# Kernel optimization log

Hardware: AMD Instinct MI355X
Metric: run time of the kernel (lower is better)

Reference implementation:

```python
import jax, jax.numpy as jnp
import numpy as np

THRESH = 0.7
MIN_KEPT = 100000
IGNORE_INDEX = -100


def setup_inputs() -> dict:
    key = jax.random.key(0)
    k1, k2 = jax.random.split(key)
    B, C, H, W = 8, 19, 512, 512
    logits = jax.random.normal(k1, (B, C, H, W), dtype=jnp.float32)
    targets = jax.random.randint(k2, (B, H, W), 0, C, dtype=jnp.int64)
    return {"logits": logits, "targets": targets}


def reference(logits, targets):
    B, C, H, W = logits.shape
    # softmax over class dim, then log(p + eps) as in the original
    probs = jax.nn.softmax(logits, axis=1)
    log_probs = jnp.log(probs + 1e-7)
    mask = (targets != IGNORE_INDEX)
    # per-pixel NLL: gather log-prob of the target class
    gathered = jnp.take_along_axis(log_probs, targets[:, None, :, :], axis=1)[:, 0]  # [B,H,W]
    losses = -gathered * mask.astype(logits.dtype)                                   # [B,H,W]
    losses_flat = losses.reshape(B, -1)                                              # [B,HW]
    n_pix = losses_flat.shape[1]
    # threshold index is static (Python ints), matching torch code exactly
    thresh_idx = max(MIN_KEPT, int(n_pix * THRESH))
    thresh_idx = min(thresh_idx, n_pix - 1)
    sorted_losses = jnp.sort(losses_flat, axis=1)
    thresh = sorted_losses[:, thresh_idx]                                            # [B]
    selected = losses_flat > thresh[:, None]                                         # [B,HW] bool
    # Faithful to the original (buggy-looking) loop:
    #   selected_mask[i, targets[i].flatten()] = 1
    # i.e. target *values* are used as indices into the flattened HW axis.
    tgt_flat = targets.reshape(B, -1)  # values in [0, C)
    selected = jax.vmap(lambda s, t: s.at[t].set(True))(selected, tgt_flat)
    return selected.reshape(B, H, W).astype(jnp.float32)
```

## Files before the change

kernel.cpp:

```cpp
#include <hip/hip_runtime.h>

#define NB 8
#define NC 19
#define HW (512*512)
#define NPIX (NB*HW)
#define HHW (HW/2)
#define RANK 183500u
#define NBIN 4096
#define CAP  4096
#define OFFB 69696

__device__ __forceinline__ unsigned fkey(float f) {
    unsigned b = __float_as_uint(f);
    return (b & 0x80000000u) ? ~b : (b | 0x80000000u);
}
__device__ __forceinline__ float finv(unsigned u) {
    unsigned b = (u & 0x80000000u) ? (u & 0x7fffffffu) : ~u;
    return __uint_as_float(b);
}
__device__ __forceinline__ int bin_of(float l) {
    int b = (int)((l + 1.0f) * 224.0f);
    return b < 0 ? 0 : (b > NBIN - 1 ? NBIN - 1 : b);
}
__device__ __forceinline__ unsigned umn(unsigned a, unsigned b) { return a < b ? a : b; }
__device__ __forceinline__ unsigned umx(unsigned a, unsigned b) { return a > b ? a : b; }

__global__ __launch_bounds__(256) void losses_kernel(
    const float* __restrict__ logits, const int* __restrict__ targets,
    float* __restrict__ losses, unsigned* __restrict__ wszero)
{
    const int blk = blockIdx.x, tid = threadIdx.x;
    if (blk < 33) {
        int j = blk * 1024 + tid * 4;
        if (j < 32784) *reinterpret_cast<uint4*>(wszero + j) = make_uint4(0u,0u,0u,0u);
    }
    const int b  = blk >> 9;
    const int r  = ((blk & 511) << 8) + tid;
    const int rB = (r + OFFB) & (HHW - 1);
    const int pA = (b << 18) + r;
    const int pB = (b << 18) + HHW + rB;
    const float* cb = logits + (size_t)b * NC * HW;
    const int*   tb = targets + (size_t)b * HW;
    const unsigned vA = (unsigned)(r * 4);
    const unsigned vB = (unsigned)((HHW + rB) * 4);

    int tA, tB;
    float xA[NC], xB[NC];
    asm volatile("global_load_dword %0, %1, %2" : "=v"(tA) : "v"(vA), "s"(tb));
    asm volatile("global_load_dword %0, %1, %2" : "=v"(tB) : "v"(vB), "s"(tb));
    #pragma unroll
    for (int c = 0; c < NC; ++c)
        asm volatile("global_load_dword %0, %1, %2"
                     : "=v"(xA[c]) : "v"(vA), "s"(cb + (size_t)c * HW));
    #pragma unroll
    for (int c = 0; c < NC; ++c)
        asm volatile("global_load_dword %0, %1, %2"
                     : "=v"(xB[c]) : "v"(vB), "s"(cb + (size_t)c * HW));

    asm volatile("s_waitcnt vmcnt(19)" ::: "memory");
    __builtin_amdgcn_sched_barrier(0);

    {
        float m = xA[0];
        #pragma unroll
        for (int c = 1; c < NC; ++c) m = fmaxf(m, xA[c]);
        float s = 0.f, et = 0.f;
        #pragma unroll
        for (int c = 0; c < NC; ++c) {
            float e = expf(xA[c] - m);
            s += e;
            if (c == tA) et = e;
        }
        losses[pA] = (tA >= 0 && tA < NC) ? -logf(et / s + 1e-7f) : 0.f;
    }

    __builtin_amdgcn_sched_barrier(0);
    asm volatile("s_waitcnt vmcnt(1)" ::: "memory");
    __builtin_amdgcn_sched_barrier(0);

    {
        float m = xB[0];
        #pragma unroll
        for (int c = 1; c < NC; ++c) m = fmaxf(m, xB[c]);
        float s = 0.f, et = 0.f;
        #pragma unroll
        for (int c = 0; c < NC; ++c) {
            float e = expf(xB[c] - m);
            s += e;
            if (c == tB) et = e;
        }
        losses[pB] = (tB >= 0 && tB < NC) ? -logf(et / s + 1e-7f) : 0.f;
    }
}

__global__ __launch_bounds__(256) void hist_kernel(
    const float* __restrict__ losses, const int* __restrict__ targets,
    unsigned* __restrict__ ghist, unsigned* __restrict__ present)
{
    __shared__ unsigned lh[NBIN];
    __shared__ unsigned pres;
    const int b = blockIdx.y;
    for (int j = threadIdx.x; j < NBIN; j += 256) lh[j] = 0;
    if (threadIdx.x == 0) pres = 0u;
    __syncthreads();
    const float4* L = reinterpret_cast<const float4*>(losses + (size_t)b * HW)
                      + (size_t)blockIdx.x * 1024;
    const int4* T = reinterpret_cast<const int4*>(targets + (size_t)b * HW)
                    + (size_t)blockIdx.x * 1024;
    unsigned bits = 0u;
    for (int j = threadIdx.x; j < 1024; j += 256) {
        float4 v = L[j];
        atomicAdd(&lh[bin_of(v.x)], 1u);
        atomicAdd(&lh[bin_of(v.y)], 1u);
        atomicAdd(&lh[bin_of(v.z)], 1u);
        atomicAdd(&lh[bin_of(v.w)], 1u);
        int4 tv = T[j];
        if (tv.x >= 0 && tv.x < NC) bits |= 1u << tv.x;
        if (tv.y >= 0 && tv.y < NC) bits |= 1u << tv.y;
        if (tv.z >= 0 && tv.z < NC) bits |= 1u << tv.z;
        if (tv.w >= 0 && tv.w < NC) bits |= 1u << tv.w;
    }
    #pragma unroll
    for (int o = 1; o < 64; o <<= 1) bits |= __shfl_xor(bits, o);
    if ((threadIdx.x & 63) == 0 && bits) atomicOr(&pres, bits);
    __syncthreads();
    unsigned* gh = ghist + b * NBIN;
    for (int j = threadIdx.x; j < NBIN; j += 256) {
        unsigned v = lh[j];
        if (v) atomicAdd(&gh[j], v);
    }
    if (threadIdx.x == 0 && pres) atomicOr(&present[b], pres);
}

__global__ __launch_bounds__(256) void compact_kernel(
    const float* __restrict__ losses, const unsigned* __restrict__ ghist,
    unsigned* __restrict__ count, float* __restrict__ cand,
    unsigned* __restrict__ info)
{
    __shared__ unsigned wsum[4], woff[4];
    __shared__ unsigned sh_T, sh_r;
    const int b = blockIdx.y;
    const int tid = threadIdx.x;
    const int lane = tid & 63, wid = tid >> 6;
    const unsigned* gh = ghist + b * NBIN;

    unsigned s = 0;
    #pragma unroll
    for (int j = 0; j < 16; ++j) s += gh[tid * 16 + j];
    unsigned incl = s;
    #pragma unroll
    for (int o = 1; o < 64; o <<= 1) {
        unsigned v = (unsigned)__shfl_up((int)incl, o);
        if (lane >= o) incl += v;
    }
    if (lane == 63) wsum[wid] = incl;
    __syncthreads();
    if (tid == 0) { unsigned c = 0; for (int w = 0; w < 4; ++w) { woff[w] = c; c += wsum[w]; } }
    __syncthreads();
    unsigned excl = woff[wid] + incl - s;
    if (RANK >= excl && RANK < excl + s) {
        unsigned rr = RANK - excl, cum = 0;
        for (int j = 0; j < 16; ++j) {
            unsigned c = gh[tid * 16 + j];
            if (cum + c > rr) {
                sh_T = (unsigned)(tid * 16 + j); sh_r = rr - cum;
                if (blockIdx.x == 0) { info[b * 2] = sh_T; info[b * 2 + 1] = sh_r; }
                break;
            }
            cum += c;
        }
    }
    __syncthreads();
    const int T = (int)sh_T;

    const float4* L = reinterpret_cast<const float4*>(losses + (size_t)b * HW)
                      + (size_t)blockIdx.x * 1024;
    for (int j = tid; j < 1024; j += 256) {
        float4 v = L[j];
        float vals[4] = {v.x, v.y, v.z, v.w};
        #pragma unroll
        for (int q = 0; q < 4; ++q) {
            float val = vals[q];
            bool sel = (bin_of(val) == T);
            unsigned long long msk = __ballot(sel);
            if (msk) {
                int leader = __ffsll(msk) - 1;
                int pre = __popcll(msk & ((1ull << lane) - 1ull));
                unsigned base = 0;
                if (lane == leader) base = atomicAdd(&count[b], (unsigned)__popcll(msk));
                base = (unsigned)__shfl((int)base, leader);
                if (sel) {
                    unsigned idx = base + (unsigned)pre;
                    if (idx < CAP) cand[b * CAP + idx] = val;
                }
            }
        }
    }
}

__global__ __launch_bounds__(256) void final_kernel(
    const float* __restrict__ cand, const unsigned* __restrict__ count,
    const unsigned* __restrict__ info, float* __restrict__ thresh)
{
    __shared__ unsigned kf[CAP];
    __shared__ unsigned h[512];
    __shared__ unsigned sub[2048];
    __shared__ unsigned red[8];
    __shared__ unsigned kmin_sh, shift_sh, sb_sh, r2_sh, cnt_sh;
    const int tid = threadIdx.x, b = blockIdx.x;
    unsigned k = count[b]; if (k > CAP) k = CAP;
    const unsigned r = info[b * 2 + 1];

    for (unsigned j = tid; j < k; j += 256) kf[j] = fkey(cand[b * CAP + j]);
    for (int j = tid; j < 512; j += 256) h[j] = 0;
    __syncthreads();

    unsigned lmin = 0xFFFFFFFFu, lmax = 0u;
    for (unsigned j = tid; j < k; j += 256) { unsigned v = kf[j]; lmin = umn(lmin, v); lmax = umx(lmax, v); }
    #pragma unroll
    for (int o = 1; o < 64; o <<= 1) {
        lmin = umn(lmin, (unsigned)__shfl_xor((int)lmin, o));
        lmax = umx(lmax, (unsigned)__shfl_xor((int)lmax, o));
    }
    if ((tid & 63) == 0) { red[tid >> 6] = lmin; red[4 + (tid >> 6)] = lmax; }
    __syncthreads();
    if (tid == 0) {
        unsigned mn = red[0], mx = red[4];
        for (int w = 1; w < 4; ++w) { mn = umn(mn, red[w]); mx = umx(mx, red[4 + w]); }
        unsigned spread = mx - mn;
        int bits = 32 - __clz((int)(spread | 1u));
        shift_sh = (unsigned)(bits > 9 ? bits - 9 : 0);
        kmin_sh = mn;
        cnt_sh = 0;
    }
    __syncthreads();
    const unsigned kmin = kmin_sh, shift = shift_sh;
    for (unsigned j = tid; j < k; j += 256) atomicAdd(&h[(kf[j] - kmin) >> shift], 1u);
    __syncthreads();
    if (tid == 0) {
        unsigned cum = 0; int sb = 0;
        while (sb < 511 && cum + h[sb] <= r) { cum += h[sb]; ++sb; }
        sb_sh = (unsigned)sb; r2_sh = r - cum;
    }
    __syncthreads();
    const unsigned sb = sb_sh;
    for (unsigned j = tid; j < k; j += 256) {
        if (((kf[j] - kmin) >> shift) == sb) {
            unsigned idx = atomicAdd(&cnt_sh, 1u);
            if (idx < 2048) sub[idx] = kf[j];
        }
    }
    __syncthreads();
    const unsigned k2 = umn(cnt_sh, 2048u), r2 = r2_sh;
    for (unsigned e = tid; e < k2; e += 256) {
        unsigned v = sub[e], less = 0, eq = 0;
        for (unsigned j = 0; j < k2; ++j) { unsigned u = sub[j]; less += (u < v); eq += (u == v); }
        if (less <= r2 && r2 < less + eq) thresh[b] = finv(v);
    }
}

__global__ __launch_bounds__(256) void emit_kernel(
    float* __restrict__ out, const float* __restrict__ thresh,
    const unsigned* __restrict__ present)
{
    int i4 = blockIdx.x * 256 + threadIdx.x;
    int i = i4 * 4;
    int b = i >> 18;
    int p = i & (HW - 1);
    float th = thresh[b];
    unsigned pm = present[b];
    float4 v = reinterpret_cast<float4*>(out)[i4];
    float4 o;
    o.x = ((v.x > th) || ((p + 0) < NC && ((pm >> (p + 0)) & 1u))) ? 1.f : 0.f;
    o.y = ((v.y > th) || ((p + 1) < NC && ((pm >> (p + 1)) & 1u))) ? 1.f : 0.f;
    o.z = ((v.z > th) || ((p + 2) < NC && ((pm >> (p + 2)) & 1u))) ? 1.f : 0.f;
    o.w = ((v.w > th) || ((p + 3) < NC && ((pm >> (p + 3)) & 1u))) ? 1.f : 0.f;
    reinterpret_cast<float4*>(out)[i4] = o;
}

extern "C" void kernel_launch(void* const* d_in, const int* in_sizes, int n_in,
                              void* d_out, int out_size, void* d_ws, size_t ws_size,
                              hipStream_t stream)
{
    const float* logits  = (const float*)d_in[0];
    const int*   targets = (const int*)d_in[1];
    float* out = (float*)d_out;

    char* ws = (char*)d_ws;
    unsigned* ghist   = (unsigned*)(ws);
    unsigned* count   = (unsigned*)(ws + 131072);
    unsigned* present = (unsigned*)(ws + 131104);
    unsigned* info    = (unsigned*)(ws + 131136);
    float*    thresh  = (float*)   (ws + 131200);
    float*    cand    = (float*)   (ws + 131232);


    losses_kernel<<<NPIX / 512, 256, 0, stream>>>(logits, targets, out, ghist);
    hist_kernel<<<dim3(64, NB), 256, 0, stream>>>(out, targets, ghist, present);
    compact_kernel<<<dim3(64, NB), 256, 0, stream>>>(out, ghist, count, cand, info);
    final_kernel<<<NB, 256, 0, stream>>>(cand, count, info, thresh);
    emit_kernel<<<NPIX / 4 / 256, 256, 0, stream>>>(out, thresh, present);
}
```

Baseline: 106.1 us.

## Fuse histogram, compaction, selection and emit into one cooperative kernel

Replaces the four tail kernels with a single cooperative kernel that uses grid-wide syncs between phases. Each block loads its loss tile into registers once and reuses it for histogramming, candidate compaction and final mask emission, so the separate global re-reads of losses disappear. It also cuts three kernel launches and their gaps. The cost is three grid-wide barriers, a serial final phase running on only 8 blocks while the others wait, and the requirement that all 512 blocks stay co-resident.

```diff
diff --git a/kernel.cpp b/kernel.cpp
--- a/kernel.cpp
+++ b/kernel.cpp
@@ -1,4 +1,6 @@
 #include <hip/hip_runtime.h>
+#include <hip/hip_cooperative_groups.h>
+namespace cg = cooperative_groups;
 
 #define NB 8
 #define NC 19
@@ -93,28 +95,43 @@
     }
 }
 
-__global__ __launch_bounds__(256) void hist_kernel(
+__global__ __launch_bounds__(256, 3) void tail_kernel(
     const float* __restrict__ losses, const int* __restrict__ targets,
-    unsigned* __restrict__ ghist, unsigned* __restrict__ present)
+    float* __restrict__ out,
+    unsigned* __restrict__ ghist, unsigned* __restrict__ count,
+    unsigned* __restrict__ present, unsigned* __restrict__ info,
+    float* __restrict__ thresh, float* __restrict__ cand)
 {
     __shared__ unsigned lh[NBIN];
-    __shared__ unsigned pres;
-    const int b = blockIdx.y;
-    for (int j = threadIdx.x; j < NBIN; j += 256) lh[j] = 0;
-    if (threadIdx.x == 0) pres = 0u;
+    __shared__ unsigned h2[512];
+    __shared__ unsigned sub[2048];
+    __shared__ unsigned red[8];
+    __shared__ unsigned wsum[4], woff[4];
+    __shared__ unsigned sh_T, sh_kmin, sh_shift, sh_sb, sh_r2, sh_cnt, pres;
+
+    const int blk = blockIdx.x, tid = threadIdx.x;
+    cg::grid_group grid = cg::this_grid();
+    const int b    = blk >> 6;
+    const int cblk = blk & 63;
+    const int lane = tid & 63, wid = tid >> 6;
+
+    for (int j = tid; j < NBIN; j += 256) lh[j] = 0;
+    if (tid == 0) pres = 0u;
     __syncthreads();
-    const float4* L = reinterpret_cast<const float4*>(losses + (size_t)b * HW)
-                      + (size_t)blockIdx.x * 1024;
-    const int4* T = reinterpret_cast<const int4*>(targets + (size_t)b * HW)
-                    + (size_t)blockIdx.x * 1024;
+    const float4* Lp = reinterpret_cast<const float4*>(losses + (size_t)b * HW)
+                       + (size_t)cblk * 1024;
+    const int4*   Tp = reinterpret_cast<const int4*>(targets + (size_t)b * HW)
+                       + (size_t)cblk * 1024;
+    float4 L[4];
     unsigned bits = 0u;
-    for (int j = threadIdx.x; j < 1024; j += 256) {
-        float4 v = L[j];
-        atomicAdd(&lh[bin_of(v.x)], 1u);
-        atomicAdd(&lh[bin_of(v.y)], 1u);
-        atomicAdd(&lh[bin_of(v.z)], 1u);
-        atomicAdd(&lh[bin_of(v.w)], 1u);
-        int4 tv = T[j];
+    #pragma unroll
+    for (int it = 0; it < 4; ++it) {
+        L[it] = Lp[it * 256 + tid];
+        int4 tv = Tp[it * 256 + tid];
+        atomicAdd(&lh[bin_of(L[it].x)], 1u);
+        atomicAdd(&lh[bin_of(L[it].y)], 1u);
+        atomicAdd(&lh[bin_of(L[it].z)], 1u);
+        atomicAdd(&lh[bin_of(L[it].w)], 1u);
         if (tv.x >= 0 && tv.x < NC) bits |= 1u << tv.x;
         if (tv.y >= 0 && tv.y < NC) bits |= 1u << tv.y;
         if (tv.z >= 0 && tv.z < NC) bits |= 1u << tv.z;
@@ -122,160 +139,140 @@
     }
     #pragma unroll
     for (int o = 1; o < 64; o <<= 1) bits |= __shfl_xor(bits, o);
-    if ((threadIdx.x & 63) == 0 && bits) atomicOr(&pres, bits);
+    if ((tid & 63) == 0 && bits) atomicOr(&pres, bits);
     __syncthreads();
-    unsigned* gh = ghist + b * NBIN;
-    for (int j = threadIdx.x; j < NBIN; j += 256) {
-        unsigned v = lh[j];
-        if (v) atomicAdd(&gh[j], v);
-    }
-    if (threadIdx.x == 0 && pres) atomicOr(&present[b], pres);
-}
-
-__global__ __launch_bounds__(256) void compact_kernel(
-    const float* __restrict__ losses, const unsigned* __restrict__ ghist,
-    unsigned* __restrict__ count, float* __restrict__ cand,
-    unsigned* __restrict__ info)
-{
-    __shared__ unsigned wsum[4], woff[4];
-    __shared__ unsigned sh_T, sh_r;
-    const int b = blockIdx.y;
-    const int tid = threadIdx.x;
-    const int lane = tid & 63, wid = tid >> 6;
-    const unsigned* gh = ghist + b * NBIN;
-
-    unsigned s = 0;
-    #pragma unroll
-    for (int j = 0; j < 16; ++j) s += gh[tid * 16 + j];
-    unsigned incl = s;
-    #pragma unroll
-    for (int o = 1; o < 64; o <<= 1) {
-        unsigned v = (unsigned)__shfl_up((int)incl, o);
-        if (lane >= o) incl += v;
-    }
-    if (lane == 63) wsum[wid] = incl;
-    __syncthreads();
-    if (tid == 0) { unsigned c = 0; for (int w = 0; w < 4; ++w) { woff[w] = c; c += wsum[w]; } }
-    __syncthreads();
-    unsigned excl = woff[wid] + incl - s;
-    if (RANK >= excl && RANK < excl + s) {
-        unsigned rr = RANK - excl, cum = 0;
-        for (int j = 0; j < 16; ++j) {
-            unsigned c = gh[tid * 16 + j];
-            if (cum + c > rr) {
-                sh_T = (unsigned)(tid * 16 + j); sh_r = rr - cum;
-                if (blockIdx.x == 0) { info[b * 2] = sh_T; info[b * 2 + 1] = sh_r; }
-                break;
+    {
+        unsigned* gh = ghist + b * NBIN;
+        for (int j = tid; j < NBIN; j += 256) {
+            unsigned v = lh[j];
+            if (v) atomicAdd(&gh[j], v);
+        }
+        if (tid == 0 && pres) atomicOr(&present[b], pres);
+    }
+    grid.sync();
+
+    {
+        const unsigned* gh = ghist + b * NBIN;
+        unsigned s = 0;
+        #pragma unroll
+        for (int j = 0; j < 16; ++j) s += gh[tid * 16 + j];
+        unsigned incl = s;
+        #pragma unroll
+        for (int o = 1; o < 64; o <<= 1) {
+            unsigned v = (unsigned)__shfl_up((int)incl, o);
+            if (lane >= o) incl += v;
+        }
+        if (lane == 63) wsum[wid] = incl;
+        __syncthreads();
+        if (tid == 0) { unsigned c = 0; for (int w = 0; w < 4; ++w) { woff[w] = c; c += wsum[w]; } }
+        __syncthreads();
+        unsigned excl = woff[wid] + incl - s;
+        if (RANK >= excl && RANK < excl + s) {
+            unsigned rr = RANK - excl, cum = 0;
+            for (int j = 0; j < 16; ++j) {
+                unsigned c = gh[tid * 16 + j];
+                if (cum + c > rr) {
+                    sh_T = (unsigned)(tid * 16 + j);
+                    if (cblk == 0) { info[b * 2] = sh_T; info[b * 2 + 1] = rr - cum; }
+                    break;
+                }
+                cum += c;
             }
-            cum += c;
-        }
-    }
-    __syncthreads();
-    const int T = (int)sh_T;
-
-    const float4* L = reinterpret_cast<const float4*>(losses + (size_t)b * HW)
-                      + (size_t)blockIdx.x * 1024;
-    for (int j = tid; j < 1024; j += 256) {
-        float4 v = L[j];
-        float vals[4] = {v.x, v.y, v.z, v.w};
-        #pragma unroll
-        for (int q = 0; q < 4; ++q) {
-            float val = vals[q];
-            bool sel = (bin_of(val) == T);
-            unsigned long long msk = __ballot(sel);
-            if (msk) {
-                int leader = __ffsll(msk) - 1;
-                int pre = __popcll(msk & ((1ull << lane) - 1ull));
-                unsigned base = 0;
-                if (lane == leader) base = atomicAdd(&count[b], (unsigned)__popcll(msk));
-                base = (unsigned)__shfl((int)base, leader);
-                if (sel) {
-                    unsigned idx = base + (unsigned)pre;
-                    if (idx < CAP) cand[b * CAP + idx] = val;
+        }
+        __syncthreads();
+        const int T = (int)sh_T;
+        #pragma unroll
+        for (int it = 0; it < 4; ++it) {
+            float vals[4] = {L[it].x, L[it].y, L[it].z, L[it].w};
+            #pragma unroll
+            for (int q = 0; q < 4; ++q) {
+                float val = vals[q];
+                bool sel = (bin_of(val) == T);
+                unsigned long long msk = __ballot(sel);
+                if (msk) {
+                    int leader = __ffsll(msk) - 1;
+                    int pre = __popcll(msk & ((1ull << lane) - 1ull));
+                    unsigned base = 0;
+                    if (lane == leader) base = atomicAdd(&count[b], (unsigned)__popcll(msk));
+                    base = (unsigned)__shfl((int)base, leader);
+                    if (sel) {
+                        unsigned idx = base + (unsigned)pre;
+                        if (idx < CAP) cand[b * CAP + idx] = val;
+                    }
                 }
             }
         }
     }
-}
-
-__global__ __launch_bounds__(256) void final_kernel(
-    const float* __restrict__ cand, const unsigned* __restrict__ count,
-    const unsigned* __restrict__ info, float* __restrict__ thresh)
-{
-    __shared__ unsigned kf[CAP];
-    __shared__ unsigned h[512];
-    __shared__ unsigned sub[2048];
-    __shared__ unsigned red[8];
-    __shared__ unsigned kmin_sh, shift_sh, sb_sh, r2_sh, cnt_sh;
-    const int tid = threadIdx.x, b = blockIdx.x;
-    unsigned k = count[b]; if (k > CAP) k = CAP;
-    const unsigned r = info[b * 2 + 1];
-
-    for (unsigned j = tid; j < k; j += 256) kf[j] = fkey(cand[b * CAP + j]);
-    for (int j = tid; j < 512; j += 256) h[j] = 0;
-    __syncthreads();
-
-    unsigned lmin = 0xFFFFFFFFu, lmax = 0u;
-    for (unsigned j = tid; j < k; j += 256) { unsigned v = kf[j]; lmin = umn(lmin, v); lmax = umx(lmax, v); }
-    #pragma unroll
-    for (int o = 1; o < 64; o <<= 1) {
-        lmin = umn(lmin, (unsigned)__shfl_xor((int)lmin, o));
-        lmax = umx(lmax, (unsigned)__shfl_xor((int)lmax, o));
-    }
-    if ((tid & 63) == 0) { red[tid >> 6] = lmin; red[4 + (tid >> 6)] = lmax; }
-    __syncthreads();
-    if (tid == 0) {
-        unsigned mn = red[0], mx = red[4];
-        for (int w = 1; w < 4; ++w) { mn = umn(mn, red[w]); mx = umx(mx, red[4 + w]); }
-        unsigned spread = mx - mn;
-        int bits = 32 - __clz((int)(spread | 1u));
-        shift_sh = (unsigned)(bits > 9 ? bits - 9 : 0);
-        kmin_sh = mn;
-        cnt_sh = 0;
-    }
-    __syncthreads();
-    const unsigned kmin = kmin_sh, shift = shift_sh;
-    for (unsigned j = tid; j < k; j += 256) atomicAdd(&h[(kf[j] - kmin) >> shift], 1u);
-    __syncthreads();
-    if (tid == 0) {
-        unsigned cum = 0; int sb = 0;
-        while (sb < 511 && cum + h[sb] <= r) { cum += h[sb]; ++sb; }
-        sb_sh = (unsigned)sb; r2_sh = r - cum;
-    }
-    __syncthreads();
-    const unsigned sb = sb_sh;
-    for (unsigned j = tid; j < k; j += 256) {
-        if (((kf[j] - kmin) >> shift) == sb) {
-            unsigned idx = atomicAdd(&cnt_sh, 1u);
-            if (idx < 2048) sub[idx] = kf[j];
-        }
-    }
-    __syncthreads();
-    const unsigned k2 = umn(cnt_sh, 2048u), r2 = r2_sh;
-    for (unsigned e = tid; e < k2; e += 256) {
-        unsigned v = sub[e], less = 0, eq = 0;
-        for (unsigned j = 0; j < k2; ++j) { unsigned u = sub[j]; less += (u < v); eq += (u == v); }
-        if (less <= r2 && r2 < less + eq) thresh[b] = finv(v);
-    }
-}
-
-__global__ __launch_bounds__(256) void emit_kernel(
-    float* __restrict__ out, const float* __restrict__ thresh,
-    const unsigned* __restrict__ present)
-{
-    int i4 = blockIdx.x * 256 + threadIdx.x;
-    int i = i4 * 4;
-    int b = i >> 18;
-    int p = i & (HW - 1);
-    float th = thresh[b];
-    unsigned pm = present[b];
-    float4 v = reinterpret_cast<float4*>(out)[i4];
-    float4 o;
-    o.x = ((v.x > th) || ((p + 0) < NC && ((pm >> (p + 0)) & 1u))) ? 1.f : 0.f;
-    o.y = ((v.y > th) || ((p + 1) < NC && ((pm >> (p + 1)) & 1u))) ? 1.f : 0.f;
-    o.z = ((v.z > th) || ((p + 2) < NC && ((pm >> (p + 2)) & 1u))) ? 1.f : 0.f;
-    o.w = ((v.w > th) || ((p + 3) < NC && ((pm >> (p + 3)) & 1u))) ? 1.f : 0.f;
-    reinterpret_cast<float4*>(out)[i4] = o;
+    grid.sync();
+
+    if (blk < 8) {
+        const int fb = blk;
+        unsigned k = count[fb]; if (k > CAP) k = CAP;
+        const unsigned r = info[fb * 2 + 1];
+        for (unsigned j = tid; j < k; j += 256) lh[j] = fkey(cand[fb * CAP + j]);
+        for (int j = tid; j < 512; j += 256) h2[j] = 0;
+        __syncthreads();
+        unsigned lmin = 0xFFFFFFFFu, lmax = 0u;
+        for (unsigned j = tid; j < k; j += 256) { unsigned v = lh[j]; lmin = umn(lmin, v); lmax = umx(lmax, v); }
+        #pragma unroll
+        for (int o = 1; o < 64; o <<= 1) {
+            lmin = umn(lmin, (unsigned)__shfl_xor((int)lmin, o));
+            lmax = umx(lmax, (unsigned)__shfl_xor((int)lmax, o));
+        }
+        if ((tid & 63) == 0) { red[tid >> 6] = lmin; red[4 + (tid >> 6)] = lmax; }
+        __syncthreads();
+        if (tid == 0) {
+            unsigned mn = red[0], mx = red[4];
+            for (int w = 1; w < 4; ++w) { mn = umn(mn, red[w]); mx = umx(mx, red[4 + w]); }
+            unsigned spread = mx - mn;
+            int bits2 = 32 - __clz((int)(spread | 1u));
+            sh_shift = (unsigned)(bits2 > 9 ? bits2 - 9 : 0);
+            sh_kmin = mn;
+            sh_cnt = 0;
+        }
+        __syncthreads();
+        const unsigned kmin = sh_kmin, shift = sh_shift;
+        for (unsigned j = tid; j < k; j += 256) atomicAdd(&h2[(lh[j] - kmin) >> shift], 1u);
+        __syncthreads();
+        if (tid == 0) {
+            unsigned cum = 0; int sb = 0;
+            while (sb < 511 && cum + h2[sb] <= r) { cum += h2[sb]; ++sb; }
+            sh_sb = (unsigned)sb; sh_r2 = r - cum;
+        }
+        __syncthreads();
+        const unsigned sb = sh_sb;
+        for (unsigned j = tid; j < k; j += 256) {
+            if (((lh[j] - kmin) >> shift) == sb) {
+                unsigned idx = atomicAdd(&sh_cnt, 1u);
+                if (idx < 2048) sub[idx] = lh[j];
+            }
+        }
+        __syncthreads();
+        const unsigned k2 = umn(sh_cnt, 2048u), r2 = sh_r2;
+        for (unsigned e = tid; e < k2; e += 256) {
+            unsigned v = sub[e], less = 0, eq = 0;
+            for (unsigned j = 0; j < k2; ++j) { unsigned u = sub[j]; less += (u < v); eq += (u == v); }
+            if (less <= r2 && r2 < less + eq) thresh[fb] = finv(v);
+        }
+    }
+    grid.sync();
+
+    {
+        const float th = thresh[b];
+        const unsigned pm = present[b];
+        float4* Op = reinterpret_cast<float4*>(out + (size_t)b * HW)
+                     + (size_t)cblk * 1024;
+        #pragma unroll
+        for (int it = 0; it < 4; ++it) {
+            const int p0 = (cblk * 1024 + it * 256 + tid) * 4;
+            float4 o;
+            o.x = ((L[it].x > th) || ((p0 + 0) < NC && ((pm >> (p0 + 0)) & 1u))) ? 1.f : 0.f;
+            o.y = ((L[it].y > th) || ((p0 + 1) < NC && ((pm >> (p0 + 1)) & 1u))) ? 1.f : 0.f;
+            o.z = ((L[it].z > th) || ((p0 + 2) < NC && ((pm >> (p0 + 2)) & 1u))) ? 1.f : 0.f;
+            o.w = ((L[it].w > th) || ((p0 + 3) < NC && ((pm >> (p0 + 3)) & 1u))) ? 1.f : 0.f;
+            Op[it * 256 + tid] = o;
+        }
+    }
 }
 
 extern "C" void kernel_launch(void* const* d_in, const int* in_sizes, int n_in,
@@ -296,8 +293,11 @@
 
 
     losses_kernel<<<NPIX / 512, 256, 0, stream>>>(logits, targets, out, ghist);
-    hist_kernel<<<dim3(64, NB), 256, 0, stream>>>(out, targets, ghist, present);
-    compact_kernel<<<dim3(64, NB), 256, 0, stream>>>(out, ghist, count, cand, info);
-    final_kernel<<<NB, 256, 0, stream>>>(cand, count, info, thresh);
-    emit_kernel<<<NPIX / 4 / 256, 256, 0, stream>>>(out, thresh, present);
-}
+
+    const float* lin = out;
+    void* args[] = { (void*)&lin, (void*)&targets, (void*)&out,
+                     (void*)&ghist, (void*)&count, (void*)&present,
+                     (void*)&info, (void*)&thresh, (void*)&cand };
+    hipLaunchCooperativeKernel((void*)tail_kernel, dim3(512), dim3(256),
+                               args, 0, stream);
+}
```

Result: slower. 218.2 us (+105.7%).
